# Kernel tuning notes

Hardware: AMD Instinct MI355X
Metric: run time of the kernel (lower is better)

The kernel has to match this reference:

```python
import jax, jax.numpy as jnp
import numpy as np
from jax import lax

V, E, NL, NS, DC, EX = 32000, 1024, 4, 16, 4, 2
DI = EX * E          # 2048 inner dim
DTR = E // 16        # 64 dt_rank
BSZ, L = 2, 512
EPS = 1e-5


def setup_inputs() -> dict:
    key = jax.random.key(0)
    ks = jax.random.split(key, 12)
    s = 0.02
    emb = jax.random.normal(ks[0], (V, E), jnp.float32) * s
    ln_w = jnp.ones((NL, E), jnp.float32)
    ln_b = jnp.zeros((NL, E), jnp.float32)
    in_proj_w = jax.random.normal(ks[1], (NL, 2 * DI, E), jnp.float32) * s
    conv_w = jax.random.normal(ks[2], (NL, DI, DC), jnp.float32) * 0.1
    conv_b = jnp.zeros((NL, DI), jnp.float32)
    x_proj_w = jax.random.normal(ks[3], (NL, DTR + 2 * NS, DI), jnp.float32) * s
    dt_proj_w = jax.random.normal(ks[4], (NL, DI, DTR), jnp.float32) * s
    dt_proj_b = jax.random.normal(ks[5], (NL, DI), jnp.float32) * 0.1
    # canonical S4D-real init: A[d,n] = n+1  ->  A_log = log(A)
    A_log = jnp.log(jnp.tile(jnp.arange(1, NS + 1, dtype=jnp.float32)[None, None, :], (NL, DI, 1)))
    D_param = jnp.ones((NL, DI), jnp.float32)
    out_proj_w = jax.random.normal(ks[6], (NL, E, DI), jnp.float32) * s
    fln_w = jnp.ones((E,), jnp.float32)
    fln_b = jnp.zeros((E,), jnp.float32)
    input_ids = jax.random.randint(ks[7], (BSZ, L), 0, V, jnp.int64)
    targets = jax.random.randint(ks[8], (BSZ, L), 0, V, jnp.int64)
    return dict(input_ids=input_ids, targets=targets, emb=emb, ln_w=ln_w, ln_b=ln_b,
                in_proj_w=in_proj_w, conv_w=conv_w, conv_b=conv_b, x_proj_w=x_proj_w,
                dt_proj_w=dt_proj_w, dt_proj_b=dt_proj_b, A_log=A_log, D_param=D_param,
                out_proj_w=out_proj_w, fln_w=fln_w, fln_b=fln_b)


def _layer_norm(x, w, b):
    mu = x.mean(-1, keepdims=True)
    var = ((x - mu) ** 2).mean(-1, keepdims=True)
    return (x - mu) * lax.rsqrt(var + EPS) * w + b


def _mamba_block(x, in_w, cw, cb, xw, dtw, dtb, a_log, d_par, ow):
    # x: (B,L,E)
    xz = jnp.einsum('ble,fe->blf', x, in_w)          # (B,L,2*DI)
    u, res = jnp.split(xz, 2, axis=-1)               # each (B,L,DI)
    # causal depthwise conv1d, kernel width DC (left pad DC-1)
    u_pad = jnp.pad(u, ((0, 0), (DC - 1, 0), (0, 0)))
    u_conv = sum(cw[:, k] * u_pad[:, k:k + u.shape[1], :] for k in range(DC))
    u = jax.nn.silu(u_conv + cb)
    x_dbl = jnp.einsum('bld,fd->blf', u, xw)         # (B,L,DTR+2*NS)
    dt = x_dbl[..., :DTR]
    Bm = x_dbl[..., DTR:DTR + NS]                    # (B,L,NS)
    Cm = x_dbl[..., DTR + NS:]                       # (B,L,NS)
    delta = jax.nn.softplus(jnp.einsum('blr,dr->bld', dt, dtw) + dtb)  # (B,L,DI)
    A = -jnp.exp(a_log)                              # (DI,NS)
    dA = jnp.exp(delta[..., None] * A)               # (B,L,DI,NS)
    dBu = delta[..., None] * Bm[:, :, None, :] * u[..., None]

    def step(h, inp):
        dA_t, dBu_t, C_t = inp
        h = dA_t * h + dBu_t                         # (B,DI,NS)
        y = jnp.einsum('bdn,bn->bd', h, C_t)
        return h, y

    h0 = jnp.zeros((x.shape[0], DI, NS), x.dtype)
    _, ys = lax.scan(step, h0, (dA.transpose(1, 0, 2, 3), dBu.transpose(1, 0, 2, 3), Cm.transpose(1, 0, 2)))
    y = ys.transpose(1, 0, 2) + u * d_par            # (B,L,DI)
    y = y * jax.nn.silu(res)
    return jnp.einsum('bld,ed->ble', y, ow)


def reference(input_ids, targets, emb, ln_w, ln_b, in_proj_w, conv_w, conv_b,
              x_proj_w, dt_proj_w, dt_proj_b, A_log, D_param, out_proj_w, fln_w, fln_b):
    x = emb[input_ids]                               # (B,L,E)
    for l in range(NL):
        h = _layer_norm(x, ln_w[l], ln_b[l])
        h = _mamba_block(h, in_proj_w[l], conv_w[l], conv_b[l], x_proj_w[l],
                         dt_proj_w[l], dt_proj_b[l], A_log[l], D_param[l], out_proj_w[l])
        x = x + h
    x = _layer_norm(x, fln_w, fln_b)
    logits = jnp.einsum('ble,ve->blv', x, emb)       # tied lm_head
    logp = jax.nn.log_softmax(logits, axis=-1)
    valid = targets != -1
    safe_t = jnp.where(valid, targets, 0)
    nll = -jnp.take_along_axis(logp, safe_t[..., None], axis=-1)[..., 0]
    loss = jnp.where(valid, nll, 0.0).mean()
    return logits, loss
```

## Files before the change

kernel.cpp:

```cpp
#include <hip/hip_runtime.h>
#include <cstdint>
#include <cstddef>

#define L_SEQ 512
#define NBATCH 2
#define NTOK 1024
#define E_DIM 1024
#define V_DIM 32000
#define DI_DIM 2048
#define NS_DIM 16
#define DTR_DIM 64
#define DC_DIM 4
#define NL_DIM 4
#define NC 8
#define LC (L_SEQ / NC)
#define CB_LOG 250

typedef __bf16 bf16;
typedef __bf16 bf16x8 __attribute__((ext_vector_type(8)));
typedef __bf16 bf16x4 __attribute__((ext_vector_type(4)));
typedef float  f32x4  __attribute__((ext_vector_type(4)));

__device__ __forceinline__ void gload_lds16(const void* g, void* l)
{
    __builtin_amdgcn_global_load_lds((const __attribute__((address_space(1))) uint32_t*)g,
                                     (__attribute__((address_space(3))) uint32_t*)l, 16, 0, 0);
}

__device__ __forceinline__ float softplusf(float z)
{
    return fmaxf(z, 0.0f) + log1pf(expf(-fabsf(z)));
}

__global__ void cast_f32_to_bf16(const float* __restrict__ in, bf16* __restrict__ out, int n4)
{
    int stride = gridDim.x * blockDim.x;
    for (int i = blockIdx.x * blockDim.x + threadIdx.x; i < n4; i += stride) {
        f32x4 v = ((const f32x4*)in)[i];
        bf16x4 o;
        o[0] = (bf16)v[0]; o[1] = (bf16)v[1]; o[2] = (bf16)v[2]; o[3] = (bf16)v[3];
        ((bf16x4*)out)[i] = o;
    }
}

__global__ void cast2_kernel(const float* __restrict__ a, bf16* __restrict__ oa, int na4,
                             const float* __restrict__ b, bf16* __restrict__ ob, int nb4)
{
    int stride = gridDim.x * blockDim.x;
    int tot = na4 + nb4;
    for (int i = blockIdx.x * blockDim.x + threadIdx.x; i < tot; i += stride) {
        const float* src; bf16* dst; int k = i;
        if (k < na4) { src = a; dst = oa; }
        else { k -= na4; src = b; dst = ob; }
        f32x4 v = ((const f32x4*)src)[k];
        bf16x4 o;
        o[0] = (bf16)v[0]; o[1] = (bf16)v[1]; o[2] = (bf16)v[2]; o[3] = (bf16)v[3];
        ((bf16x4*)dst)[k] = o;
    }
}

__global__ void embed_kernel(const int* __restrict__ ids, const float* __restrict__ emb,
                             float* __restrict__ x)
{
    int t = blockIdx.x;
    int id = ids[t];
    ((f32x4*)(x + (size_t)t * E_DIM))[threadIdx.x] =
        ((const f32x4*)(emb + (size_t)id * E_DIM))[threadIdx.x];
}

__global__ void ln_kernel(const float* __restrict__ x, const float* __restrict__ w,
                          const float* __restrict__ b, bf16* __restrict__ out)
{
    int t = blockIdx.x;
    int tid = threadIdx.x;
    f32x4 v = ((const f32x4*)(x + (size_t)t * E_DIM))[tid];
    float s  = v[0] + v[1] + v[2] + v[3];
    float sq = v[0]*v[0] + v[1]*v[1] + v[2]*v[2] + v[3]*v[3];
#pragma unroll
    for (int off = 1; off < 64; off <<= 1) { s += __shfl_xor(s, off); sq += __shfl_xor(sq, off); }
    __shared__ float ps[4], pq[4];
    if ((tid & 63) == 0) { ps[tid >> 6] = s; pq[tid >> 6] = sq; }
    __syncthreads();
    float S  = ps[0] + ps[1] + ps[2] + ps[3];
    float SQ = pq[0] + pq[1] + pq[2] + pq[3];
    float mu  = S * (1.0f / E_DIM);
    float var = SQ * (1.0f / E_DIM) - mu * mu;
    float rs  = rsqrtf(var + 1e-5f);
    f32x4 wv = ((const f32x4*)w)[tid];
    f32x4 bv = ((const f32x4*)b)[tid];
    bf16x4 o;
#pragma unroll
    for (int i = 0; i < 4; ++i) o[i] = (bf16)((v[i] - mu) * rs * wv[i] + bv[i]);
    ((bf16x4*)(out + (size_t)t * E_DIM))[tid] = o;
}

template<int BM, int BN, int MODE>
__global__ __launch_bounds__(256) void gemm_bt(const bf16* __restrict__ A, const bf16* __restrict__ B,
                                               float* __restrict__ C, int K,
                                               int lda, int ldb, int ldc,
                                               float* __restrict__ Pm, float* __restrict__ Ps,
                                               int RB, int CB, int CBpad)
{
    int pid = blockIdx.x;
    int xcd = pid & 7;
    int j   = pid >> 3;
    int cpx = CBpad >> 3;
    int rb  = j % RB;
    int cb  = xcd * cpx + j / RB;
    if (cb >= CB) return;

    __shared__ __align__(16) bf16 As[BM * 32];
    __shared__ __align__(16) bf16 Bs[BN * 32];
    int tid  = threadIdx.x;
    int lane = tid & 63;
    int wid  = tid >> 6;
    int wr = wid >> 1, wc = wid & 1;
    int li = lane & 15, lg = lane >> 4;
    const bf16* Ablk = A + (size_t)(rb * BM) * lda;
    const bf16* Bblk = B + (size_t)(cb * BN) * ldb;
    constexpr int MR  = BM / 32;
    constexpr int NR  = BN / 32;
    constexpr int TOT = (BM + BN) * 4;
    f32x4 acc[MR][NR] = {};
    for (int k0 = 0; k0 < K; k0 += 32) {
        __syncthreads();
#pragma unroll
        for (int it = 0; it < TOT / 256; ++it) {
            int wbase = it * 256 + wid * 64;
            int idx   = wbase + lane;
            if (wbase < BM * 4) {
                int row = idx >> 2, seg = idx & 3;
                gload_lds16(Ablk + (size_t)row * lda + k0 + seg * 8, As + (size_t)wbase * 8);
            } else {
                int bb  = wbase - BM * 4;
                int bi  = bb + lane;
                int row = bi >> 2, seg = bi & 3;
                gload_lds16(Bblk + (size_t)row * ldb + k0 + seg * 8, Bs + (size_t)bb * 8);
            }
        }
        __syncthreads();
        bf16x8 af[MR], bfr[NR];
#pragma unroll
        for (int m = 0; m < MR; ++m) af[m]  = *(const bf16x8*)&As[(wr * (BM/2) + m * 16 + li) * 32 + lg * 8];
#pragma unroll
        for (int n = 0; n < NR; ++n) bfr[n] = *(const bf16x8*)&Bs[(wc * (BN/2) + n * 16 + li) * 32 + lg * 8];
#pragma unroll
        for (int m = 0; m < MR; ++m)
#pragma unroll
            for (int n = 0; n < NR; ++n)
                acc[m][n] = __builtin_amdgcn_mfma_f32_16x16x32_bf16(af[m], bfr[n], acc[m][n], 0, 0, 0);
    }
    int row0 = rb * BM + wr * (BM/2);
    int col0 = cb * BN + wc * (BN/2);
#pragma unroll
    for (int m = 0; m < MR; ++m) {
#pragma unroll
        for (int n = 0; n < NR; ++n) {
            int r = row0 + m * 16 + lg * 4;
            int c = col0 + n * 16 + li;
            float* cp = C + (size_t)r * ldc + c;
#pragma unroll
            for (int q = 0; q < 4; ++q) {
                float v = acc[m][n][q];
                if (MODE == 1) v += cp[(size_t)q * ldc];
                cp[(size_t)q * ldc] = v;
            }
        }
    }
    if constexpr (MODE == 3) {
        __shared__ float lm_s[2][2][BM / 2], ls_s[2][2][BM / 2];
#pragma unroll
        for (int m = 0; m < MR; ++m) {
#pragma unroll
            for (int q = 0; q < 4; ++q) {
                float mx = acc[m][0][q];
#pragma unroll
                for (int n = 1; n < NR; ++n) mx = fmaxf(mx, acc[m][n][q]);
#pragma unroll
                for (int off = 1; off < 16; off <<= 1) mx = fmaxf(mx, __shfl_xor(mx, off));
                float sv = 0.0f;
#pragma unroll
                for (int n = 0; n < NR; ++n) sv += __expf(acc[m][n][q] - mx);
#pragma unroll
                for (int off = 1; off < 16; off <<= 1) sv += __shfl_xor(sv, off);
                if (li == 0) {
                    int rl = m * 16 + lg * 4 + q;
                    lm_s[wr][wc][rl] = mx;
                    ls_s[wr][wc][rl] = sv;
                }
            }
        }
        __syncthreads();
        if (tid < BM) {
            int wrh = tid >> 6, rl = tid & 63;
            float m0 = lm_s[wrh][0][rl], m1 = lm_s[wrh][1][rl];
            float M  = fmaxf(m0, m1);
            float S  = ls_s[wrh][0][rl] * __expf(m0 - M) + ls_s[wrh][1][rl] * __expf(m1 - M);
            size_t r = (size_t)(rb * BM + tid);
            Pm[r * 256 + cb] = M;
            Ps[r * 256 + cb] = S;
        }
    }
}

template<int BM, int BN, int MODE>
static void launch_gemm(const bf16* A, const bf16* B, float* C, int M, int N, int K,
                        int lda, int ldb, int ldc, float* Pm, float* Ps, hipStream_t stream)
{
    int RB = M / BM;
    int CB = (N + BN - 1) / BN;
    int CBpad = (CB + 7) & ~7;
    gemm_bt<BM, BN, MODE><<<RB * CBpad, 256, 0, stream>>>(A, B, C, K, lda, ldb, ldc, Pm, Ps, RB, CB, CBpad);
}

__global__ __launch_bounds__(256) void cxk_kernel(
        const float* __restrict__ xz, const float* __restrict__ cw,
        const float* __restrict__ cb, const float* __restrict__ xw,
        float* __restrict__ xdbl, bf16* __restrict__ dt_bf, bf16* __restrict__ u_bf)
{
    int t0  = blockIdx.x * 4;
    int bb  = t0 >> 9;
    int tid = threadIdx.x;
    int f   = tid & 127;
    int ks  = tid >> 7;
    __shared__ __align__(16) float sxz[7][256];
    __shared__ __align__(16) float su[4][256];
    __shared__ float pacc[4][128];
    float acc[4] = {0, 0, 0, 0};
    for (int kc = 0; kc < DI_DIM; kc += 256) {
        __syncthreads();
#pragma unroll
        for (int i = 0; i < 2; ++i) {
            int idx = i * 256 + tid;
            if (idx < 448) {
                int row = idx >> 6, c4 = (idx & 63) * 4;
                int tr = t0 - 3 + row;
                f32x4 v = {0, 0, 0, 0};
                if (tr >= bb * L_SEQ)
                    v = *(const f32x4*)&xz[(size_t)tr * (2 * DI_DIM) + kc + c4];
                *(f32x4*)&sxz[row][c4] = v;
            }
        }
        __syncthreads();
        {
            int c = tid;
            const float* cwp = cw + (size_t)(kc + c) * DC_DIM;
            float w0 = cwp[0], w1 = cwp[1], w2 = cwp[2], w3 = cwp[3];
            float bs = cb[kc + c];
#pragma unroll
            for (int tt = 0; tt < 4; ++tt) {
                float a = bs + w0 * sxz[tt][c] + w1 * sxz[tt + 1][c]
                             + w2 * sxz[tt + 2][c] + w3 * sxz[tt + 3][c];
                float uo = a / (1.0f + __expf(-a));
                su[tt][c] = uo;
                u_bf[(size_t)(t0 + tt) * DI_DIM + kc + c] = (bf16)uo;
            }
        }
        __syncthreads();
        if (f < 96) {
            int kb = ks * 128;
            for (int kk = kb; kk < kb + 128; kk += 4) {
                f32x4 wv = *(const f32x4*)&xw[(size_t)f * DI_DIM + kc + kk];
#pragma unroll
                for (int tt = 0; tt < 4; ++tt) {
                    f32x4 uv = *(f32x4*)&su[tt][kk];
                    acc[tt] += wv[0]*uv[0] + wv[1]*uv[1] + wv[2]*uv[2] + wv[3]*uv[3];
                }
            }
        }
    }
    if (ks == 1 && f < 96) {
#pragma unroll
        for (int tt = 0; tt < 4; ++tt) pacc[tt][f] = acc[tt];
    }
    __syncthreads();
    if (ks == 0 && f < 96) {
#pragma unroll
        for (int tt = 0; tt < 4; ++tt) {
            float v = acc[tt] + pacc[tt][f];
            xdbl[(size_t)(t0 + tt) * 96 + f] = v;
            if (f < 64) dt_bf[(size_t)(t0 + tt) * DTR_DIM + f] = (bf16)v;
        }
    }
}

__global__ __launch_bounds__(256) void scan_phase_a(
        const bf16* __restrict__ dt_g, const float* __restrict__ dtw,
        const float* __restrict__ dtb, const float* __restrict__ xdbl,
        const bf16* __restrict__ u_bf, const float* __restrict__ A_log,
        float* __restrict__ Pbuf, float* __restrict__ Sbuf)
{
    int tid = threadIdx.x;
    int c   = blockIdx.x & (NC - 1);
    int dblk= (blockIdx.x >> 3) & 127;
    int b   = blockIdx.x >> 10;
    int d0  = dblk << 4;
    int n = tid & 15, dl = tid >> 4;
    int d = d0 + dl;
    float Ac = -expf(A_log[(size_t)d * NS_DIM + n]);
    float h = 0.0f, P = 1.0f;
    __shared__ float s_dt[32][65];
    __shared__ float s_dtw[16][64];
    __shared__ float s_dtb[16];
    __shared__ float s_dlt[32][17];
    __shared__ float s_u[32][16], s_B[32][16];
    {
        int idx = tid * 4;
        int rowD = idx >> 6, c4 = idx & 63;
        *(f32x4*)&s_dtw[rowD][c4] = *(const f32x4*)&dtw[(size_t)(d0 + rowD) * DTR_DIM + c4];
        if (tid < 16) s_dtb[tid] = dtb[d0 + tid];
    }
    int tt0 = tid >> 4, cc = tid & 15;
    int tbase = b * L_SEQ + c * LC;
    for (int t0 = 0; t0 < LC; t0 += 32) {
        __syncthreads();
        {
            int row = tid >> 3, c8 = (tid & 7) * 8;
            bf16x8 v = *(const bf16x8*)&dt_g[(size_t)(tbase + t0 + row) * DTR_DIM + c8];
#pragma unroll
            for (int jj = 0; jj < 8; ++jj) s_dt[row][c8 + jj] = (float)v[jj];
        }
#pragma unroll
        for (int jj = 0; jj < 2; ++jj) {
            int tt = jj * 16 + tt0;
            size_t trow = (size_t)(tbase + t0 + tt);
            s_u[tt][cc] = (float)u_bf[trow * DI_DIM + d0 + cc];
            s_B[tt][cc] = xdbl[trow * 96 + 64 + cc];
        }
        __syncthreads();
        {
            int td = tid & 31, dd = tid >> 5;
            float a0 = s_dtb[dd], a1 = s_dtb[dd + 8];
#pragma unroll
            for (int k = 0; k < 64; ++k) {
                float a = s_dt[td][k];
                a0 = fmaf(a, s_dtw[dd][k], a0);
                a1 = fmaf(a, s_dtw[dd + 8][k], a1);
            }
            s_dlt[td][dd]     = softplusf(a0);
            s_dlt[td][dd + 8] = softplusf(a1);
        }
        __syncthreads();
#pragma unroll
        for (int t = 0; t < 32; ++t) {
            float dlt = s_dlt[t][dl];
            float dA  = __expf(dlt * Ac);
            h = fmaf(dA, h, dlt * s_B[t][n] * s_u[t][dl]);
            P *= dA;
        }
    }
    size_t oi = (((size_t)(b * NC + c) * DI_DIM) + d) * NS_DIM + n;
    Pbuf[oi] = P;
    Sbuf[oi] = h;
}

__global__ void scan_combine(const float* __restrict__ Pbuf, const float* __restrict__ Sbuf,
                             float* __restrict__ Hstart)
{
    int i  = blockIdx.x * 256 + threadIdx.x;
    int b  = i >> 15;
    int dn = i & 32767;
    float h = 0.0f;
#pragma unroll
    for (int c = 0; c < NC; ++c) {
        size_t oi = ((size_t)(b * NC + c) * (DI_DIM * NS_DIM)) + dn;
        Hstart[oi] = h;
        h = fmaf(Pbuf[oi], h, Sbuf[oi]);
    }
}

__global__ __launch_bounds__(256) void scan_phase_c(
        const bf16* __restrict__ dt_g, const float* __restrict__ dtw,
        const float* __restrict__ dtb, const float* __restrict__ xdbl,
        const bf16* __restrict__ u_bf, const float* __restrict__ xz,
        const float* __restrict__ A_log, const float* __restrict__ D_par,
        const float* __restrict__ Hstart, bf16* __restrict__ y)
{
    int tid = threadIdx.x;
    int c   = blockIdx.x & (NC - 1);
    int dblk= (blockIdx.x >> 3) & 127;
    int b   = blockIdx.x >> 10;
    int d0  = dblk << 4;
    int n = tid & 15, dl = tid >> 4;
    int d = d0 + dl;
    float Ac = -expf(A_log[(size_t)d * NS_DIM + n]);
    float Dp = D_par[d];
    float h = Hstart[(((size_t)(b * NC + c) * DI_DIM) + d) * NS_DIM + n];
    __shared__ float s_dt[32][65];
    __shared__ float s_dtw[16][64];
    __shared__ float s_dtb[16];
    __shared__ float s_dlt[32][17];
    __shared__ float s_u[32][16], s_res[32][16], s_B[32][16], s_C[32][16];
    __shared__ bf16  s_y[32][16];
    {
        int idx = tid * 4;
        int rowD = idx >> 6, c4 = idx & 63;
        *(f32x4*)&s_dtw[rowD][c4] = *(const f32x4*)&dtw[(size_t)(d0 + rowD) * DTR_DIM + c4];
        if (tid < 16) s_dtb[tid] = dtb[d0 + tid];
    }
    int tt0 = tid >> 4, cc = tid & 15;
    int tbase = b * L_SEQ + c * LC;
    for (int t0 = 0; t0 < LC; t0 += 32) {
        __syncthreads();
        {
            int row = tid >> 3, c8 = (tid & 7) * 8;
            bf16x8 v = *(const bf16x8*)&dt_g[(size_t)(tbase + t0 + row) * DTR_DIM + c8];
#pragma unroll
            for (int jj = 0; jj < 8; ++jj) s_dt[row][c8 + jj] = (float)v[jj];
        }
#pragma unroll
        for (int jj = 0; jj < 2; ++jj) {
            int tt = jj * 16 + tt0;
            size_t trow = (size_t)(tbase + t0 + tt);
            s_u[tt][cc]   = (float)u_bf[trow * DI_DIM + d0 + cc];
            s_res[tt][cc] = xz[trow * (2 * DI_DIM) + DI_DIM + d0 + cc];
            s_B[tt][cc]   = xdbl[trow * 96 + 64 + cc];
            s_C[tt][cc]   = xdbl[trow * 96 + 80 + cc];
        }
        __syncthreads();
        {
            int td = tid & 31, dd = tid >> 5;
            float a0 = s_dtb[dd], a1 = s_dtb[dd + 8];
#pragma unroll
            for (int k = 0; k < 64; ++k) {
                float a = s_dt[td][k];
                a0 = fmaf(a, s_dtw[dd][k], a0);
                a1 = fmaf(a, s_dtw[dd + 8][k], a1);
            }
            s_dlt[td][dd]     = softplusf(a0);
            s_dlt[td][dd + 8] = softplusf(a1);
        }
        __syncthreads();
#pragma unroll
        for (int t = 0; t < 32; ++t) {
            float dlt = s_dlt[t][dl];
            float uu  = s_u[t][dl];
            float dA  = __expf(dlt * Ac);
            float dBu = dlt * s_B[t][n] * uu;
            h = fmaf(dA, h, dBu);
            float yp = h * s_C[t][n];
            yp += __shfl_xor(yp, 1);
            yp += __shfl_xor(yp, 2);
            yp += __shfl_xor(yp, 4);
            yp += __shfl_xor(yp, 8);
            if (n == 0) {
                float res = s_res[t][dl];
                float yv  = fmaf(uu, Dp, yp) * (res / (1.0f + __expf(-res)));
                s_y[t][dl] = (bf16)yv;
            }
        }
        __syncthreads();
#pragma unroll
        for (int jj = 0; jj < 2; ++jj) {
            int tt = jj * 16 + tt0;
            size_t trow = (size_t)(tbase + t0 + tt);
            y[trow * DI_DIM + d0 + cc] = s_y[tt][cc];
        }
    }
}

__global__ void lse_fin_kernel(const float* __restrict__ Pm, const float* __restrict__ Ps,
                               const float* __restrict__ logits, const int* __restrict__ targets,
                               float* __restrict__ nll)
{
    int t = blockIdx.x, tid = threadIdx.x;
    float m = -1e30f, s = 0.0f;
    for (int i = tid; i < CB_LOG; i += 256) {
        float mo = Pm[(size_t)t * 256 + i], so = Ps[(size_t)t * 256 + i];
        float nm = fmaxf(m, mo);
        s = s * __expf(m - nm) + so * __expf(mo - nm);
        m = nm;
    }
#pragma unroll
    for (int off = 1; off < 64; off <<= 1) {
        float mo = __shfl_xor(m, off), so = __shfl_xor(s, off);
        float nm = fmaxf(m, mo);
        s = s * __expf(m - nm) + so * __expf(mo - nm);
        m = nm;
    }
    __shared__ float pm[4], ps2[4];
    if ((tid & 63) == 0) { pm[tid >> 6] = m; ps2[tid >> 6] = s; }
    __syncthreads();
    if (tid == 0) {
        float M = fmaxf(fmaxf(pm[0], pm[1]), fmaxf(pm[2], pm[3]));
        float S = ps2[0] * __expf(pm[0] - M) + ps2[1] * __expf(pm[1] - M)
                + ps2[2] * __expf(pm[2] - M) + ps2[3] * __expf(pm[3] - M);
        int tg = targets[t];
        float v = 0.0f;
        if (tg >= 0) v = (M + logf(S)) - logits[(size_t)t * V_DIM + tg];
        nll[t] = v;
    }
}

__global__ void loss_reduce_kernel(const float* __restrict__ nll, float* __restrict__ out)
{
    int tid = threadIdx.x;
    float s = 0.0f;
    for (int i = tid; i < NTOK; i += 256) s += nll[i];
#pragma unroll
    for (int off = 1; off < 64; off <<= 1) s += __shfl_xor(s, off);
    __shared__ float p[4];
    if ((tid & 63) == 0) p[tid >> 6] = s;
    __syncthreads();
    if (tid == 0) out[0] = (p[0] + p[1] + p[2] + p[3]) * (1.0f / NTOK);
}

extern "C" void kernel_launch(void* const* d_in, const int* in_sizes, int n_in,
                              void* d_out, int out_size, void* d_ws, size_t ws_size,
                              hipStream_t stream)
{
    const int*   ids   = (const int*)d_in[0];
    const int*   tgt   = (const int*)d_in[1];
    const float* emb   = (const float*)d_in[2];
    const float* ln_w  = (const float*)d_in[3];
    const float* ln_b  = (const float*)d_in[4];
    const float* inw   = (const float*)d_in[5];
    const float* convw = (const float*)d_in[6];
    const float* convb = (const float*)d_in[7];
    const float* xw    = (const float*)d_in[8];
    const float* dtw   = (const float*)d_in[9];
    const float* dtb   = (const float*)d_in[10];
    const float* alog  = (const float*)d_in[11];
    const float* dpar  = (const float*)d_in[12];
    const float* outw  = (const float*)d_in[13];
    const float* flnw  = (const float*)d_in[14];
    const float* flnb  = (const float*)d_in[15];
    float* logits = (float*)d_out;
    float* lossp  = logits + (size_t)NTOK * V_DIM;

    char* wsp = (char*)d_ws;
    size_t off = 0;
    auto alloc = [&](size_t bytes) -> void* {
        void* p = wsp + off;
        off += (bytes + 255) & ~(size_t)255;
        return p;
    };
    bf16*  emb_bf  = (bf16*)alloc((size_t)V_DIM * E_DIM * 2);
    bf16*  winl    = (bf16*)alloc((size_t)2 * DI_DIM * E_DIM * 2);
    bf16*  woutl   = (bf16*)alloc((size_t)E_DIM * DI_DIM * 2);
    float* x       = (float*)alloc((size_t)NTOK * E_DIM * 4);
    bf16*  h_bf    = (bf16*)alloc((size_t)NTOK * E_DIM * 2);
    float* xzb     = (float*)alloc((size_t)NTOK * 2 * DI_DIM * 4);
    bf16*  u_bf    = (bf16*)alloc((size_t)NTOK * DI_DIM * 2);
    float* xdbl    = (float*)alloc((size_t)NTOK * 96 * 4);
    bf16*  dt_bf   = (bf16*)alloc((size_t)NTOK * DTR_DIM * 2);
    bf16*  y_bf    = (bf16*)alloc((size_t)NTOK * DI_DIM * 2);
    bf16*  xf_bf   = (bf16*)alloc((size_t)NTOK * E_DIM * 2);
    float* nll     = (float*)alloc((size_t)NTOK * 4);
    float* Pbuf    = (float*)alloc((size_t)NBATCH * NC * DI_DIM * NS_DIM * 4);
    float* Sbuf    = (float*)alloc((size_t)NBATCH * NC * DI_DIM * NS_DIM * 4);
    float* Hstart  = (float*)alloc((size_t)NBATCH * NC * DI_DIM * NS_DIM * 4);
    float* Pm      = (float*)alloc((size_t)NTOK * 256 * 4);
    float* Ps      = (float*)alloc((size_t)NTOK * 256 * 4);
    if (off > ws_size) return;

    {
        int n4 = (int)((size_t)V_DIM * E_DIM / 4);
        cast_f32_to_bf16<<<4096, 256, 0, stream>>>(emb, emb_bf, n4);
    }
    embed_kernel<<<NTOK, 256, 0, stream>>>(ids, emb, x);

    for (int l = 0; l < NL_DIM; ++l) {
        cast2_kernel<<<2048, 256, 0, stream>>>(
            inw  + (size_t)l * 2 * DI_DIM * E_DIM, winl,  (int)((size_t)2 * DI_DIM * E_DIM / 4),
            outw + (size_t)l * E_DIM * DI_DIM,     woutl, (int)((size_t)E_DIM * DI_DIM / 4));

        ln_kernel<<<NTOK, 256, 0, stream>>>(x, ln_w + l * E_DIM, ln_b + l * E_DIM, h_bf);
        launch_gemm<128, 64, 0>(h_bf, winl, xzb, NTOK, 2 * DI_DIM, E_DIM,
                                E_DIM, E_DIM, 2 * DI_DIM, nullptr, nullptr, stream);
        cxk_kernel<<<NTOK / 4, 256, 0, stream>>>(
            xzb, convw + (size_t)l * DI_DIM * DC_DIM, convb + (size_t)l * DI_DIM,
            xw + (size_t)l * 96 * DI_DIM, xdbl, dt_bf, u_bf);
        scan_phase_a<<<NBATCH * (DI_DIM / 16) * NC, 256, 0, stream>>>(
            dt_bf, dtw + (size_t)l * DI_DIM * DTR_DIM, dtb + (size_t)l * DI_DIM,
            xdbl, u_bf, alog + (size_t)l * DI_DIM * NS_DIM, Pbuf, Sbuf);
        scan_combine<<<NBATCH * DI_DIM * NS_DIM / 256, 256, 0, stream>>>(Pbuf, Sbuf, Hstart);
        scan_phase_c<<<NBATCH * (DI_DIM / 16) * NC, 256, 0, stream>>>(
            dt_bf, dtw + (size_t)l * DI_DIM * DTR_DIM, dtb + (size_t)l * DI_DIM,
            xdbl, u_bf, xzb, alog + (size_t)l * DI_DIM * NS_DIM, dpar + (size_t)l * DI_DIM,
            Hstart, y_bf);
        launch_gemm<64, 64, 1>(y_bf, woutl, x, NTOK, E_DIM, DI_DIM,
                               DI_DIM, DI_DIM, E_DIM, nullptr, nullptr, stream);
    }
    ln_kernel<<<NTOK, 256, 0, stream>>>(x, flnw, flnb, xf_bf);
    launch_gemm<128, 128, 3>(xf_bf, emb_bf, logits, NTOK, V_DIM, E_DIM,
                             E_DIM, E_DIM, V_DIM, Pm, Ps, stream);
    lse_fin_kernel<<<NTOK, 256, 0, stream>>>(Pm, Ps, logits, tgt, nll);
    loss_reduce_kernel<<<1, 256, 0, stream>>>(nll, lossp);
}
```

Baseline: 919.9 us.

## Hoist dt_proj into MFMA GEMM, store xz in bf16, atomic loss reduction

Computes delta = softplus(dt @ dt_proj_w + b) once with a bf16 MFMA GEMM that writes bf16 output. Before this, both scan phases recomputed that product in scalar FMAs for every block. The in_proj GEMM now writes xz in bf16 instead of fp32, halving that intermediate's traffic for the conv and scan kernels. The LM-head partial LSE is written per wave, with no shared-memory combine or barrier, and the final loss uses atomicAdd in place of a separate reduce kernel. The costs are extra precision loss from the bf16 xz and delta, a new delta buffer, and a nondeterministic atomic summation order.

```diff
diff --git a/kernel.cpp b/kernel.cpp
--- a/kernel.cpp
+++ b/kernel.cpp
@@ -43,15 +43,17 @@
     }
 }
 
-__global__ void cast2_kernel(const float* __restrict__ a, bf16* __restrict__ oa, int na4,
-                             const float* __restrict__ b, bf16* __restrict__ ob, int nb4)
+__global__ void cast3_kernel(const float* __restrict__ a, bf16* __restrict__ oa, int na4,
+                             const float* __restrict__ b, bf16* __restrict__ ob, int nb4,
+                             const float* __restrict__ c, bf16* __restrict__ oc, int nc4)
 {
     int stride = gridDim.x * blockDim.x;
-    int tot = na4 + nb4;
+    int tot = na4 + nb4 + nc4;
     for (int i = blockIdx.x * blockDim.x + threadIdx.x; i < tot; i += stride) {
         const float* src; bf16* dst; int k = i;
         if (k < na4) { src = a; dst = oa; }
-        else { k -= na4; src = b; dst = ob; }
+        else if ((k -= na4) < nb4) { src = b; dst = ob; }
+        else { k -= nb4; src = c; dst = oc; }
         f32x4 v = ((const f32x4*)src)[k];
         bf16x4 o;
         o[0] = (bf16)v[0]; o[1] = (bf16)v[1]; o[2] = (bf16)v[2]; o[3] = (bf16)v[3];
@@ -96,8 +98,9 @@
 
 template<int BM, int BN, int MODE>
 __global__ __launch_bounds__(256) void gemm_bt(const bf16* __restrict__ A, const bf16* __restrict__ B,
-                                               float* __restrict__ C, int K,
+                                               void* __restrict__ Cv, int K,
                                                int lda, int ldb, int ldc,
+                                               const float* __restrict__ bias,
                                                float* __restrict__ Pm, float* __restrict__ Ps,
                                                int RB, int CB, int CBpad)
 {
@@ -152,23 +155,31 @@
     }
     int row0 = rb * BM + wr * (BM/2);
     int col0 = cb * BN + wc * (BN/2);
+    float* Cf = (float*)Cv;
+    bf16*  Cb = (bf16*)Cv;
 #pragma unroll
     for (int m = 0; m < MR; ++m) {
 #pragma unroll
         for (int n = 0; n < NR; ++n) {
             int r = row0 + m * 16 + lg * 4;
             int c = col0 + n * 16 + li;
-            float* cp = C + (size_t)r * ldc + c;
 #pragma unroll
             for (int q = 0; q < 4; ++q) {
                 float v = acc[m][n][q];
-                if (MODE == 1) v += cp[(size_t)q * ldc];
-                cp[(size_t)q * ldc] = v;
+                if (MODE == 0 || MODE == 3) {
+                    Cf[(size_t)(r + q) * ldc + c] = v;
+                } else if (MODE == 1) {
+                    float* cp = Cf + (size_t)(r + q) * ldc + c;
+                    *cp = v + *cp;
+                } else if (MODE == 2) {
+                    Cb[(size_t)(r + q) * ldc + c] = (bf16)softplusf(v + bias[c]);
+                } else if (MODE == 4) {
+                    Cb[(size_t)(r + q) * ldc + c] = (bf16)v;
+                }
             }
         }
     }
     if constexpr (MODE == 3) {
-        __shared__ float lm_s[2][2][BM / 2], ls_s[2][2][BM / 2];
 #pragma unroll
         for (int m = 0; m < MR; ++m) {
 #pragma unroll
@@ -184,37 +195,29 @@
 #pragma unroll
                 for (int off = 1; off < 16; off <<= 1) sv += __shfl_xor(sv, off);
                 if (li == 0) {
-                    int rl = m * 16 + lg * 4 + q;
-                    lm_s[wr][wc][rl] = mx;
-                    ls_s[wr][wc][rl] = sv;
+                    size_t r = (size_t)(row0 + m * 16 + lg * 4 + q);
+                    Pm[r * 512 + cb * 2 + wc] = mx;
+                    Ps[r * 512 + cb * 2 + wc] = sv;
                 }
             }
         }
-        __syncthreads();
-        if (tid < BM) {
-            int wrh = tid >> 6, rl = tid & 63;
-            float m0 = lm_s[wrh][0][rl], m1 = lm_s[wrh][1][rl];
-            float M  = fmaxf(m0, m1);
-            float S  = ls_s[wrh][0][rl] * __expf(m0 - M) + ls_s[wrh][1][rl] * __expf(m1 - M);
-            size_t r = (size_t)(rb * BM + tid);
-            Pm[r * 256 + cb] = M;
-            Ps[r * 256 + cb] = S;
-        }
     }
 }
 
 template<int BM, int BN, int MODE>
-static void launch_gemm(const bf16* A, const bf16* B, float* C, int M, int N, int K,
-                        int lda, int ldb, int ldc, float* Pm, float* Ps, hipStream_t stream)
+static void launch_gemm(const bf16* A, const bf16* B, void* C, int M, int N, int K,
+                        int lda, int ldb, int ldc, const float* bias,
+                        float* Pm, float* Ps, hipStream_t stream)
 {
     int RB = M / BM;
     int CB = (N + BN - 1) / BN;
     int CBpad = (CB + 7) & ~7;
-    gemm_bt<BM, BN, MODE><<<RB * CBpad, 256, 0, stream>>>(A, B, C, K, lda, ldb, ldc, Pm, Ps, RB, CB, CBpad);
+    gemm_bt<BM, BN, MODE><<<RB * CBpad, 256, 0, stream>>>(A, B, C, K, lda, ldb, ldc,
+                                                          bias, Pm, Ps, RB, CB, CBpad);
 }
 
 __global__ __launch_bounds__(256) void cxk_kernel(
-        const float* __restrict__ xz, const float* __restrict__ cw,
+        const bf16* __restrict__ xz, const float* __restrict__ cw,
         const float* __restrict__ cb, const float* __restrict__ xw,
         float* __restrict__ xdbl, bf16* __restrict__ dt_bf, bf16* __restrict__ u_bf)
 {
@@ -229,17 +232,17 @@
     float acc[4] = {0, 0, 0, 0};
     for (int kc = 0; kc < DI_DIM; kc += 256) {
         __syncthreads();
-#pragma unroll
-        for (int i = 0; i < 2; ++i) {
-            int idx = i * 256 + tid;
-            if (idx < 448) {
-                int row = idx >> 6, c4 = (idx & 63) * 4;
-                int tr = t0 - 3 + row;
-                f32x4 v = {0, 0, 0, 0};
-                if (tr >= bb * L_SEQ)
-                    v = *(const f32x4*)&xz[(size_t)tr * (2 * DI_DIM) + kc + c4];
-                *(f32x4*)&sxz[row][c4] = v;
-            }
+        if (tid < 224) {
+            int row = tid >> 5, c8 = (tid & 31) * 8;
+            int tr = t0 - 3 + row;
+            float vals[8] = {0, 0, 0, 0, 0, 0, 0, 0};
+            if (tr >= bb * L_SEQ) {
+                bf16x8 v = *(const bf16x8*)&xz[(size_t)tr * (2 * DI_DIM) + kc + c8];
+#pragma unroll
+                for (int jj = 0; jj < 8; ++jj) vals[jj] = (float)v[jj];
+            }
+#pragma unroll
+            for (int jj = 0; jj < 8; ++jj) sxz[row][c8 + jj] = vals[jj];
         }
         __syncthreads();
         {
@@ -285,8 +288,7 @@
 }
 
 __global__ __launch_bounds__(256) void scan_phase_a(
-        const bf16* __restrict__ dt_g, const float* __restrict__ dtw,
-        const float* __restrict__ dtb, const float* __restrict__ xdbl,
+        const bf16* __restrict__ delta, const float* __restrict__ xdbl,
         const bf16* __restrict__ u_bf, const float* __restrict__ A_log,
         float* __restrict__ Pbuf, float* __restrict__ Sbuf)
 {
@@ -299,46 +301,18 @@
     int d = d0 + dl;
     float Ac = -expf(A_log[(size_t)d * NS_DIM + n]);
     float h = 0.0f, P = 1.0f;
-    __shared__ float s_dt[32][65];
-    __shared__ float s_dtw[16][64];
-    __shared__ float s_dtb[16];
-    __shared__ float s_dlt[32][17];
-    __shared__ float s_u[32][16], s_B[32][16];
-    {
-        int idx = tid * 4;
-        int rowD = idx >> 6, c4 = idx & 63;
-        *(f32x4*)&s_dtw[rowD][c4] = *(const f32x4*)&dtw[(size_t)(d0 + rowD) * DTR_DIM + c4];
-        if (tid < 16) s_dtb[tid] = dtb[d0 + tid];
-    }
+    __shared__ float s_dlt[32][16], s_u[32][16], s_B[32][16];
     int tt0 = tid >> 4, cc = tid & 15;
     int tbase = b * L_SEQ + c * LC;
     for (int t0 = 0; t0 < LC; t0 += 32) {
         __syncthreads();
-        {
-            int row = tid >> 3, c8 = (tid & 7) * 8;
-            bf16x8 v = *(const bf16x8*)&dt_g[(size_t)(tbase + t0 + row) * DTR_DIM + c8];
-#pragma unroll
-            for (int jj = 0; jj < 8; ++jj) s_dt[row][c8 + jj] = (float)v[jj];
-        }
 #pragma unroll
         for (int jj = 0; jj < 2; ++jj) {
             int tt = jj * 16 + tt0;
             size_t trow = (size_t)(tbase + t0 + tt);
-            s_u[tt][cc] = (float)u_bf[trow * DI_DIM + d0 + cc];
-            s_B[tt][cc] = xdbl[trow * 96 + 64 + cc];
-        }
-        __syncthreads();
-        {
-            int td = tid & 31, dd = tid >> 5;
-            float a0 = s_dtb[dd], a1 = s_dtb[dd + 8];
-#pragma unroll
-            for (int k = 0; k < 64; ++k) {
-                float a = s_dt[td][k];
-                a0 = fmaf(a, s_dtw[dd][k], a0);
-                a1 = fmaf(a, s_dtw[dd + 8][k], a1);
-            }
-            s_dlt[td][dd]     = softplusf(a0);
-            s_dlt[td][dd + 8] = softplusf(a1);
+            s_dlt[tt][cc] = (float)delta[trow * DI_DIM + d0 + cc];
+            s_u[tt][cc]   = (float)u_bf[trow * DI_DIM + d0 + cc];
+            s_B[tt][cc]   = xdbl[trow * 96 + 64 + cc];
         }
         __syncthreads();
 #pragma unroll
@@ -370,9 +344,8 @@
 }
 
 __global__ __launch_bounds__(256) void scan_phase_c(
-        const bf16* __restrict__ dt_g, const float* __restrict__ dtw,
-        const float* __restrict__ dtb, const float* __restrict__ xdbl,
-        const bf16* __restrict__ u_bf, const float* __restrict__ xz,
+        const bf16* __restrict__ delta, const float* __restrict__ xdbl,
+        const bf16* __restrict__ u_bf, const bf16* __restrict__ xz,
         const float* __restrict__ A_log, const float* __restrict__ D_par,
         const float* __restrict__ Hstart, bf16* __restrict__ y)
 {
@@ -386,49 +359,21 @@
     float Ac = -expf(A_log[(size_t)d * NS_DIM + n]);
     float Dp = D_par[d];
     float h = Hstart[(((size_t)(b * NC + c) * DI_DIM) + d) * NS_DIM + n];
-    __shared__ float s_dt[32][65];
-    __shared__ float s_dtw[16][64];
-    __shared__ float s_dtb[16];
-    __shared__ float s_dlt[32][17];
-    __shared__ float s_u[32][16], s_res[32][16], s_B[32][16], s_C[32][16];
+    __shared__ float s_dlt[32][16], s_u[32][16], s_res[32][16], s_B[32][16], s_C[32][16];
     __shared__ bf16  s_y[32][16];
-    {
-        int idx = tid * 4;
-        int rowD = idx >> 6, c4 = idx & 63;
-        *(f32x4*)&s_dtw[rowD][c4] = *(const f32x4*)&dtw[(size_t)(d0 + rowD) * DTR_DIM + c4];
-        if (tid < 16) s_dtb[tid] = dtb[d0 + tid];
-    }
     int tt0 = tid >> 4, cc = tid & 15;
     int tbase = b * L_SEQ + c * LC;
     for (int t0 = 0; t0 < LC; t0 += 32) {
         __syncthreads();
-        {
-            int row = tid >> 3, c8 = (tid & 7) * 8;
-            bf16x8 v = *(const bf16x8*)&dt_g[(size_t)(tbase + t0 + row) * DTR_DIM + c8];
-#pragma unroll
-            for (int jj = 0; jj < 8; ++jj) s_dt[row][c8 + jj] = (float)v[jj];
-        }
 #pragma unroll
         for (int jj = 0; jj < 2; ++jj) {
             int tt = jj * 16 + tt0;
             size_t trow = (size_t)(tbase + t0 + tt);
+            s_dlt[tt][cc] = (float)delta[trow * DI_DIM + d0 + cc];
             s_u[tt][cc]   = (float)u_bf[trow * DI_DIM + d0 + cc];
-            s_res[tt][cc] = xz[trow * (2 * DI_DIM) + DI_DIM + d0 + cc];
+            s_res[tt][cc] = (float)xz[trow * (2 * DI_DIM) + DI_DIM + d0 + cc];
             s_B[tt][cc]   = xdbl[trow * 96 + 64 + cc];
             s_C[tt][cc]   = xdbl[trow * 96 + 80 + cc];
-        }
-        __syncthreads();
-        {
-            int td = tid & 31, dd = tid >> 5;
-            float a0 = s_dtb[dd], a1 = s_dtb[dd + 8];
-#pragma unroll
-            for (int k = 0; k < 64; ++k) {
-                float a = s_dt[td][k];
-                a0 = fmaf(a, s_dtw[dd][k], a0);
-                a1 = fmaf(a, s_dtw[dd + 8][k], a1);
-            }
-            s_dlt[td][dd]     = softplusf(a0);
-            s_dlt[td][dd + 8] = softplusf(a1);
         }
         __syncthreads();
 #pragma unroll
@@ -461,12 +406,12 @@
 
 __global__ void lse_fin_kernel(const float* __restrict__ Pm, const float* __restrict__ Ps,
                                const float* __restrict__ logits, const int* __restrict__ targets,
-                               float* __restrict__ nll)
+                               float* __restrict__ lossp)
 {
     int t = blockIdx.x, tid = threadIdx.x;
     float m = -1e30f, s = 0.0f;
-    for (int i = tid; i < CB_LOG; i += 256) {
-        float mo = Pm[(size_t)t * 256 + i], so = Ps[(size_t)t * 256 + i];
+    for (int i = tid; i < 2 * CB_LOG; i += 256) {
+        float mo = Pm[(size_t)t * 512 + i], so = Ps[(size_t)t * 512 + i];
         float nm = fmaxf(m, mo);
         s = s * __expf(m - nm) + so * __expf(mo - nm);
         m = nm;
@@ -486,23 +431,11 @@
         float S = ps2[0] * __expf(pm[0] - M) + ps2[1] * __expf(pm[1] - M)
                 + ps2[2] * __expf(pm[2] - M) + ps2[3] * __expf(pm[3] - M);
         int tg = targets[t];
-        float v = 0.0f;
-        if (tg >= 0) v = (M + logf(S)) - logits[(size_t)t * V_DIM + tg];
-        nll[t] = v;
-    }
-}
-
-__global__ void loss_reduce_kernel(const float* __restrict__ nll, float* __restrict__ out)
-{
-    int tid = threadIdx.x;
-    float s = 0.0f;
-    for (int i = tid; i < NTOK; i += 256) s += nll[i];
-#pragma unroll
-    for (int off = 1; off < 64; off <<= 1) s += __shfl_xor(s, off);
-    __shared__ float p[4];
-    if ((tid & 63) == 0) p[tid >> 6] = s;
-    __syncthreads();
-    if (tid == 0) out[0] = (p[0] + p[1] + p[2] + p[3]) * (1.0f / NTOK);
+        if (tg >= 0) {
+            float v = (M + logf(S)) - logits[(size_t)t * V_DIM + tg];
+            atomicAdd(lossp, v * (1.0f / NTOK));
+        }
+    }
 }
 
 extern "C" void kernel_launch(void* const* d_in, const int* in_sizes, int n_in,
@@ -538,22 +471,24 @@
     bf16*  emb_bf  = (bf16*)alloc((size_t)V_DIM * E_DIM * 2);
     bf16*  winl    = (bf16*)alloc((size_t)2 * DI_DIM * E_DIM * 2);
     bf16*  woutl   = (bf16*)alloc((size_t)E_DIM * DI_DIM * 2);
+    bf16*  wdtl    = (bf16*)alloc((size_t)DI_DIM * DTR_DIM * 2);
     float* x       = (float*)alloc((size_t)NTOK * E_DIM * 4);
     bf16*  h_bf    = (bf16*)alloc((size_t)NTOK * E_DIM * 2);
-    float* xzb     = (float*)alloc((size_t)NTOK * 2 * DI_DIM * 4);
+    bf16*  xzb     = (bf16*)alloc((size_t)NTOK * 2 * DI_DIM * 2);
     bf16*  u_bf    = (bf16*)alloc((size_t)NTOK * DI_DIM * 2);
     float* xdbl    = (float*)alloc((size_t)NTOK * 96 * 4);
     bf16*  dt_bf   = (bf16*)alloc((size_t)NTOK * DTR_DIM * 2);
+    bf16*  deltab  = (bf16*)alloc((size_t)NTOK * DI_DIM * 2);
     bf16*  y_bf    = (bf16*)alloc((size_t)NTOK * DI_DIM * 2);
     bf16*  xf_bf   = (bf16*)alloc((size_t)NTOK * E_DIM * 2);
-    float* nll     = (float*)alloc((size_t)NTOK * 4);
     float* Pbuf    = (float*)alloc((size_t)NBATCH * NC * DI_DIM * NS_DIM * 4);
     float* Sbuf    = (float*)alloc((size_t)NBATCH * NC * DI_DIM * NS_DIM * 4);
     float* Hstart  = (float*)alloc((size_t)NBATCH * NC * DI_DIM * NS_DIM * 4);
-    float* Pm      = (float*)alloc((size_t)NTOK * 256 * 4);
-    float* Ps      = (float*)alloc((size_t)NTOK * 256 * 4);
+    float* Pm      = (float*)alloc((size_t)NTOK * 512 * 4);
+    float* Ps      = (float*)alloc((size_t)NTOK * 512 * 4);
     if (off > ws_size) return;
 
+    hipMemsetAsync(lossp, 0, sizeof(float), stream);
     {
         int n4 = (int)((size_t)V_DIM * E_DIM / 4);
         cast_f32_to_bf16<<<4096, 256, 0, stream>>>(emb, emb_bf, n4);
@@ -561,30 +496,31 @@
     embed_kernel<<<NTOK, 256, 0, stream>>>(ids, emb, x);
 
     for (int l = 0; l < NL_DIM; ++l) {
-        cast2_kernel<<<2048, 256, 0, stream>>>(
+        cast3_kernel<<<2048, 256, 0, stream>>>(
             inw  + (size_t)l * 2 * DI_DIM * E_DIM, winl,  (int)((size_t)2 * DI_DIM * E_DIM / 4),
-            outw + (size_t)l * E_DIM * DI_DIM,     woutl, (int)((size_t)E_DIM * DI_DIM / 4));
+            outw + (size_t)l * E_DIM * DI_DIM,     woutl, (int)((size_t)E_DIM * DI_DIM / 4),
+            dtw  + (size_t)l * DI_DIM * DTR_DIM,   wdtl,  (int)((size_t)DI_DIM * DTR_DIM / 4));
 
         ln_kernel<<<NTOK, 256, 0, stream>>>(x, ln_w + l * E_DIM, ln_b + l * E_DIM, h_bf);
-        launch_gemm<128, 64, 0>(h_bf, winl, xzb, NTOK, 2 * DI_DIM, E_DIM,
-                                E_DIM, E_DIM, 2 * DI_DIM, nullptr, nullptr, stream);
+        launch_gemm<128, 64, 4>(h_bf, winl, xzb, NTOK, 2 * DI_DIM, E_DIM,
+                                E_DIM, E_DIM, 2 * DI_DIM, nullptr, nullptr, nullptr, stream);
         cxk_kernel<<<NTOK / 4, 256, 0, stream>>>(
             xzb, convw + (size_t)l * DI_DIM * DC_DIM, convb + (size_t)l * DI_DIM,
             xw + (size_t)l * 96 * DI_DIM, xdbl, dt_bf, u_bf);
+        launch_gemm<64, 64, 2>(dt_bf, wdtl, deltab, NTOK, DI_DIM, DTR_DIM,
+                               DTR_DIM, DTR_DIM, DI_DIM, dtb + (size_t)l * DI_DIM,
+                               nullptr, nullptr, stream);
         scan_phase_a<<<NBATCH * (DI_DIM / 16) * NC, 256, 0, stream>>>(
-            dt_bf, dtw + (size_t)l * DI_DIM * DTR_DIM, dtb + (size_t)l * DI_DIM,
-            xdbl, u_bf, alog + (size_t)l * DI_DIM * NS_DIM, Pbuf, Sbuf);
+            deltab, xdbl, u_bf, alog + (size_t)l * DI_DIM * NS_DIM, Pbuf, Sbuf);
         scan_combine<<<NBATCH * DI_DIM * NS_DIM / 256, 256, 0, stream>>>(Pbuf, Sbuf, Hstart);
         scan_phase_c<<<NBATCH * (DI_DIM / 16) * NC, 256, 0, stream>>>(
-            dt_bf, dtw + (size_t)l * DI_DIM * DTR_DIM, dtb + (size_t)l * DI_DIM,
-            xdbl, u_bf, xzb, alog + (size_t)l * DI_DIM * NS_DIM, dpar + (size_t)l * DI_DIM,
-            Hstart, y_bf);
+            deltab, xdbl, u_bf, xzb, alog + (size_t)l * DI_DIM * NS_DIM,
+            dpar + (size_t)l * DI_DIM, Hstart, y_bf);
         launch_gemm<64, 64, 1>(y_bf, woutl, x, NTOK, E_DIM, DI_DIM,
-                               DI_DIM, DI_DIM, E_DIM, nullptr, nullptr, stream);
+                               DI_DIM, DI_DIM, E_DIM, nullptr, nullptr, nullptr, stream);
     }
     ln_kernel<<<NTOK, 256, 0, stream>>>(x, flnw, flnb, xf_bf);
     launch_gemm<128, 128, 3>(xf_bf, emb_bf, logits, NTOK, V_DIM, E_DIM,
-                             E_DIM, E_DIM, V_DIM, Pm, Ps, stream);
-    lse_fin_kernel<<<NTOK, 256, 0, stream>>>(Pm, Ps, logits, tgt, nll);
-    loss_reduce_kernel<<<1, 256, 0, stream>>>(nll, lossp);
-}
+                             E_DIM, E_DIM, V_DIM, nullptr, Pm, Ps, stream);
+    lse_fin_kernel<<<NTOK, 256, 0, stream>>>(Pm, Ps, logits, tgt, lossp);
+}
```

After: 884.9 us. -3.8%, faster.
